# Kernel tuning notes

Measured on AMD Instinct MI355X. Metric: run time of the kernel, lower is better.

## Reference

```python
import jax, jax.numpy as jnp
import numpy as np

B, T, D, H, E = 2, 1024, 1024, 4096, 8


def setup_inputs() -> dict:
    key = jax.random.key(0)
    ks = jax.random.split(key, 7)
    s = 0.02  # weight init scale
    return {
        "x": jax.random.normal(ks[0], (B, T, D), jnp.float32),
        "gate_w": jax.random.normal(ks[1], (D, E), jnp.float32) * s,
        "gate_b": jnp.zeros((E,), jnp.float32),
        "w1": jax.random.normal(ks[2], (E, D, H), jnp.float32) * s,
        "b1": jnp.zeros((E, H), jnp.float32),
        "w2": jax.random.normal(ks[3], (E, H, D), jnp.float32) * s,
        "b2": jnp.zeros((E, D), jnp.float32),
    }


def reference(x, gate_w, gate_b, w1, b1, w2, b2):
    b, t, d = x.shape
    e = gate_w.shape[1]
    xt = x.reshape(b * t, d)                      # [N, D]
    logits = xt @ gate_w + gate_b                 # [N, E]
    probs = jax.nn.softmax(logits, axis=-1)
    top_expert = jnp.argmax(probs, axis=-1)       # [N]
    onehot = jax.nn.one_hot(top_expert, e, dtype=x.dtype)  # [N, E]
    # dense per-expert FFN, then combine via top-1 one-hot (same math as masked dispatch)
    h = jax.nn.gelu(jnp.einsum('nd,edh->enh', xt, w1) + b1[:, None, :], approximate=False)  # [E, N, H]
    y = jnp.einsum('enh,ehd->end', h, w2) + b2[:, None, :]                                  # [E, N, D]
    out = jnp.einsum('end,ne->nd', y, onehot).reshape(b, t, d)
    counts = jnp.sum(onehot, axis=0)              # [E], float
    frac = counts / jnp.maximum(counts.sum(), 1.0)
    aux_loss = jnp.mean((frac - 1.0 / e) ** 2)
    return out, aux_loss
```

## Files before the change

kernel.cpp:

```cpp
#include <hip/hip_runtime.h>
#include <stdint.h>

#define N_TOK 2048
#define DDIM 1024
#define HDIM 4096
#define NEXP 8
#define BM 256
#define MAXT 16
#define ACAP 2560

#define C_COUNTS 0
#define C_CURSOR 8
#define C_PADOFF 16
#define C_TILECNT 25
#define C_TILE_E 32
#define C_TILE_M0 56
#define C_TILE_ROWS 80
#define C_EXPERT 128
#define C_PERM 2176

#define XG_OFF 32768
#define HG_OFF (XG_OFF + ACAP*DDIM*2)

typedef float f32x4 __attribute__((ext_vector_type(4)));
typedef short s16x8 __attribute__((ext_vector_type(8)));
typedef unsigned int u32;
typedef u32 u32x2 __attribute__((ext_vector_type(2)));
typedef unsigned short u16;

__device__ __forceinline__ u16 f2bf(float f){
  u32 u = __float_as_uint(f);
  u += 0x7fffu + ((u >> 16) & 1u);
  return (u16)(u >> 16);
}

__device__ __forceinline__ u32 pkbf(float a, float b){
  u32 r; asm("v_cvt_pk_bf16_f32 %0, %1, %2" : "=v"(r) : "v"(a), "v"(b)); return r;
}

__device__ __forceinline__ void gl_lds16(const void* g, void* l){
  __builtin_amdgcn_global_load_lds((const __attribute__((address_space(1))) u32*)g,
                                   (__attribute__((address_space(3))) u32*)l, 16, 0, 0);
}

__global__ __launch_bounds__(256) void gate_kern(
    const float* __restrict__ x, const float* __restrict__ gw,
    const float* __restrict__ gb, int* __restrict__ ctrl)
{
  const int wv = threadIdx.x >> 6, l = threadIdx.x & 63;
  const int n = blockIdx.x * 4 + wv;
  const float* xr = x + (size_t)n * DDIM;
  float acc[NEXP];
  #pragma unroll
  for (int e = 0; e < NEXP; e++) acc[e] = 0.f;
  #pragma unroll 4
  for (int i = 0; i < DDIM/64; i++){
    int k = i*64 + l;
    float xv = xr[k];
    const float* g = gw + (size_t)k * NEXP;
    #pragma unroll
    for (int e = 0; e < NEXP; e++) acc[e] = fmaf(xv, g[e], acc[e]);
  }
  #pragma unroll
  for (int e = 0; e < NEXP; e++){
    #pragma unroll
    for (int off = 32; off > 0; off >>= 1) acc[e] += __shfl_xor(acc[e], off);
  }
  if (l == 0){
    float best = acc[0] + gb[0]; int bi = 0;
    #pragma unroll
    for (int e = 1; e < NEXP; e++){
      float v = acc[e] + gb[e];
      if (v > best){ best = v; bi = e; }
    }
    ctrl[C_EXPERT + n] = bi;
    atomicAdd(&ctrl[C_COUNTS + bi], 1);
  }
}

__global__ void setup_kern(int* __restrict__ ctrl, float* __restrict__ aux_out)
{
  const int t = threadIdx.x;
  for (int i = t; i < 3072; i += 256) ctrl[C_PERM + i] = -1;
  if (t == 0){
    int off = 0, tc = 0;
    float aux = 0.f;
    for (int e = 0; e < NEXP; e++){
      int c = ctrl[C_COUNTS + e];
      ctrl[C_PADOFF + e] = off;
      ctrl[C_CURSOR + e] = off;
      int nt = (c + BM - 1) / BM;
      for (int j = 0; j < nt; j++){
        ctrl[C_TILE_E   + tc] = e;
        ctrl[C_TILE_M0  + tc] = off + j*BM;
        ctrl[C_TILE_ROWS+ tc] = min(BM, c - j*BM);
        tc++;
      }
      off += c;
      float fr = (float)c * (1.f/(float)N_TOK);
      float d = fr - 1.f/(float)NEXP;
      aux += d*d;
    }
    ctrl[C_TILECNT] = tc;
    *aux_out = aux * (1.f/(float)NEXP);
  }
}

__global__ __launch_bounds__(256) void scatter_kern(int* __restrict__ ctrl)
{
  const int n = blockIdx.x * 256 + threadIdx.x;
  const int e = ctrl[C_EXPERT + n];
  const int pos = atomicAdd(&ctrl[C_CURSOR + e], 1);
  ctrl[C_PERM + pos] = n;
}

__global__ __launch_bounds__(256) void xg_kern(
    const float* __restrict__ x, const int* __restrict__ ctrl,
    u16* __restrict__ Xg)
{
  const int slot = blockIdx.x, t = threadIdx.x;
  const int tok = ctrl[C_PERM + slot];
  ushort4 o;
  if (tok >= 0){
    f32x4 v = *(const f32x4*)(x + (size_t)tok*DDIM + t*4);
    o.x = f2bf(v.x); o.y = f2bf(v.y); o.z = f2bf(v.z); o.w = f2bf(v.w);
  } else { o.x = 0; o.y = 0; o.z = 0; o.w = 0; }
  *(ushort4*)(Xg + (size_t)slot*DDIM + t*4) = o;
}

template<int MODE>
__global__ __launch_bounds__(512, 2) void moe_gemm(
    const u16* __restrict__ Ag, const float* __restrict__ W,
    const float* __restrict__ bias, u16* __restrict__ Hg,
    float* __restrict__ outp, const int* __restrict__ ctrl)
{
  constexpr int K    = (MODE==1) ? DDIM : HDIM;
  constexpr int NN   = (MODE==1) ? HDIM : DDIM;
  constexpr int KS   = (MODE==1) ? 1 : 4;
  constexpr int KLOC = K / KS;
  constexpr int BN   = 128;
  constexpr int BK   = 32;
  constexpr int NT   = KLOC / BK;

  const int by = blockIdx.y;
  if (by >= ctrl[C_TILECNT]) return;
  const int e    = ctrl[C_TILE_E + by];
  const int m0   = ctrl[C_TILE_M0 + by];
  const int rows = ctrl[C_TILE_ROWS + by];
  const int n0   = blockIdx.x * BN;
  const int kb   = (MODE==1) ? 0 : blockIdx.z * KLOC;

  const int tid = threadIdx.x;
  const int w = tid >> 6, l = tid & 63;
  const int wr = w >> 1, wc = w & 1;
  const int lhi = l >> 4, llo = l & 15;

  __shared__ __align__(16) u16 As[2][BM*BK];
  __shared__ __align__(16) u16 Bs[2][BN*BK];
  __shared__ int perm_s[BM];

  if constexpr (MODE == 2){
    if (tid < BM) perm_s[tid] = ctrl[C_PERM + m0 + tid];
  }

  f32x4 acc[4][4];
  #pragma unroll
  for (int mf = 0; mf < 4; mf++)
    #pragma unroll
    for (int nf = 0; nf < 4; nf++) acc[mf][nf] = (f32x4){0.f,0.f,0.f,0.f};

  const u16* Abase = Ag + (size_t)m0 * K;
  int arow[2], apos[2];
  #pragma unroll
  for (int i = 0; i < 2; i++){
    int f = i*512 + tid;
    arow[i] = f >> 2;
    apos[i] = (f & 3) ^ (arow[i] & 3) ^ (((arow[i] >> 2) & 1) << 1);
  }
  const int bn  = tid & 127;
  const int bkg = tid >> 7;
  const int bsw = (bn >> 1) & 7;
  const float* Wn = W + (size_t)e * K * NN + n0 + bn;
  float wreg[8];

#define STAGE_A(buf, k0) { \
    u16* ad = &As[buf][(w*64)*8]; \
    _Pragma("unroll") \
    for (int i = 0; i < 2; i++) \
      gl_lds16(Abase + (size_t)arow[i]*K + (k0) + apos[i]*8, ad + i*512*8); }

#define BLOAD(k0) { \
    _Pragma("unroll") \
    for (int i = 0; i < 8; i++) \
      wreg[i] = Wn[(size_t)((k0) + bkg*8 + i) * NN]; }

#define BPACK(buf) { \
    u32 p0 = pkbf(wreg[0], wreg[1]), p1 = pkbf(wreg[2], wreg[3]); \
    u32 p2 = pkbf(wreg[4], wreg[5]), p3 = pkbf(wreg[6], wreg[7]); \
    u16* bd = &Bs[buf][bn*BK]; \
    *(u32x2*)&bd[((2*bkg)   ^ bsw) << 2] = (u32x2){p0, p1}; \
    *(u32x2*)&bd[((2*bkg+1) ^ bsw) << 2] = (u32x2){p2, p3}; }

#define COMPUTE(buf) { \
    s16x8 a[4]; \
    _Pragma("unroll") \
    for (int mf = 0; mf < 4; mf++){ \
      int row = wr*64 + mf*16 + llo; \
      int pos = (lhi ^ (row & 3)) ^ (((row >> 2) & 1) << 1); \
      a[mf] = *(const s16x8*)&As[buf][row*BK + pos*8]; } \
    _Pragma("unroll") \
    for (int nf = 0; nf < 4; nf++){ \
      const int col = wc*64 + nf*16 + llo; \
      const int sw = (col >> 1) & 7; \
      const u16* bb = &Bs[buf][col*BK]; \
      union { u32 u[4]; s16x8 v; } bfr; \
      *(u32x2*)&bfr.u[0] = *(const u32x2*)&bb[((2*lhi)   ^ sw) << 2]; \
      *(u32x2*)&bfr.u[2] = *(const u32x2*)&bb[((2*lhi+1) ^ sw) << 2]; \
      _Pragma("unroll") \
      for (int mf = 0; mf < 4; mf++) \
        acc[mf][nf] = __builtin_amdgcn_mfma_f32_16x16x32_bf16(a[mf], bfr.v, acc[mf][nf], 0, 0, 0); \
    } }

  BLOAD(kb);
  STAGE_A(0, kb);
  BPACK(0);
  __syncthreads();

  int cur = 0;
  #pragma unroll 1
  for (int t = 0; t < NT; t++){
    if (t+1 < NT){
      BLOAD(kb + (t+1)*BK);
      STAGE_A(cur^1, kb + (t+1)*BK);
    }
    COMPUTE(cur);
    if (t+1 < NT){ BPACK(cur^1); }
    __syncthreads();
    cur ^= 1;
  }

  if constexpr (MODE == 1){
    const float* bp = bias + (size_t)e*NN + n0;
    #pragma unroll
    for (int nf = 0; nf < 4; nf++){
      const int cl = wc*64 + nf*16 + llo;
      const float bb = bp[cl];
      #pragma unroll
      for (int mf = 0; mf < 4; mf++){
        #pragma unroll
        for (int r = 0; r < 4; r++){
          const int rl = wr*64 + mf*16 + lhi*4 + r;
          if (rl < rows){
            float vv = acc[mf][nf][r] + bb;
            float gel = 0.5f * vv * (1.0f + erff(vv * 0.70710678118f));
            Hg[(size_t)(m0+rl)*NN + n0 + cl] = f2bf(gel);
          }
        }
      }
    }
  } else {
    const float* bp = bias + (size_t)e*NN + n0;
    const bool addb = (blockIdx.z == 0);
    #pragma unroll
    for (int mf = 0; mf < 4; mf++){
      #pragma unroll
      for (int r = 0; r < 4; r++){
        const int rl = wr*64 + mf*16 + lhi*4 + r;
        if (rl < rows){
          const int tok = perm_s[rl];
          #pragma unroll
          for (int nf = 0; nf < 4; nf++){
            const int cl = wc*64 + nf*16 + llo;
            float v = acc[mf][nf][r] + (addb ? bp[cl] : 0.f);
            atomicAdd(&outp[(size_t)tok*DDIM + n0 + cl], v);
          }
        }
      }
    }
  }
#undef STAGE_A
#undef BLOAD
#undef BPACK
#undef COMPUTE
}

extern "C" void kernel_launch(void* const* d_in, const int* in_sizes, int n_in,
                              void* d_out, int out_size, void* d_ws, size_t ws_size,
                              hipStream_t stream)
{
  (void)in_sizes; (void)n_in; (void)out_size; (void)ws_size;
  const float* x  = (const float*)d_in[0];
  const float* gw = (const float*)d_in[1];
  const float* gb = (const float*)d_in[2];
  const float* w1 = (const float*)d_in[3];
  const float* b1 = (const float*)d_in[4];
  const float* w2 = (const float*)d_in[5];
  const float* b2 = (const float*)d_in[6];
  float* out = (float*)d_out;
  char* ws = (char*)d_ws;
  int* ctrl = (int*)ws;
  u16* Xg = (u16*)(ws + XG_OFF);
  u16* Hg = (u16*)(ws + HG_OFF);

  hipMemsetAsync(ctrl, 0, 64, stream);
  hipMemsetAsync(out, 0, (size_t)N_TOK*DDIM*4, stream);
  gate_kern<<<N_TOK/4, 256, 0, stream>>>(x, gw, gb, ctrl);
  setup_kern<<<1, 256, 0, stream>>>(ctrl, out + (size_t)N_TOK*DDIM);
  scatter_kern<<<N_TOK/256, 256, 0, stream>>>(ctrl);
  xg_kern<<<N_TOK, 256, 0, stream>>>(x, ctrl, Xg);
  moe_gemm<1><<<dim3(HDIM/128, MAXT),    512, 0, stream>>>(Xg, w1, b1, Hg, nullptr, ctrl);
  moe_gemm<2><<<dim3(DDIM/128, MAXT, 4), 512, 0, stream>>>(Hg, w2, b2, nullptr, out, ctrl);
}
```

Baseline: 216.4 us.

## Pre-convert expert weights to transposed bf16 and use 128-row GEMM tiles

Adds a kernel that converts and transposes all fp32 expert weights into bf16 in workspace every call, so the GEMMs can stream weights with direct global-to-LDS copies and no per-tile fp32-to-bf16 packing. The GEMM tile shrinks to 128 rows with BK=64 and 256 threads, giving more tiles per expert. The new path runs only when the workspace is large enough, otherwise it falls back to the old fp32-weight kernels. The conversion reads all 256 MB of fp32 weights and writes 128 MB of bf16 each call, so total weight traffic rises unless the GEMMs get much cheaper.

New measurement: 285.6 us. 32.0% more time.

```diff
diff --git a/kernel.cpp b/kernel.cpp
--- a/kernel.cpp
+++ b/kernel.cpp
@@ -5,9 +5,6 @@
 #define DDIM 1024
 #define HDIM 4096
 #define NEXP 8
-#define BM 256
-#define MAXT 16
-#define ACAP 2560
 
 #define C_COUNTS 0
 #define C_CURSOR 8
@@ -19,8 +16,16 @@
 #define C_EXPERT 128
 #define C_PERM 2176
 
-#define XG_OFF 32768
-#define HG_OFF (XG_OFF + ACAP*DDIM*2)
+#define ACAPB 2304
+#define XGB_OFF 32768
+#define HGB_OFF (XGB_OFF + ACAPB*DDIM*2)
+#define W1B_OFF (HGB_OFF + ACAPB*HDIM*2)
+#define W2B_OFF (W1B_OFF + (size_t)NEXP*DDIM*HDIM*2)
+#define WS_NEED (W2B_OFF + (size_t)NEXP*HDIM*DDIM*2)
+
+#define ACAP2 2560
+#define XG2_OFF 32768
+#define HG2_OFF (XG2_OFF + ACAP2*DDIM*2)
 
 typedef float f32x4 __attribute__((ext_vector_type(4)));
 typedef short s16x8 __attribute__((ext_vector_type(8)));
@@ -78,7 +83,8 @@
   }
 }
 
-__global__ void setup_kern(int* __restrict__ ctrl, float* __restrict__ aux_out)
+__global__ void setup_kern(int* __restrict__ ctrl, float* __restrict__ aux_out,
+                           int bm)
 {
   const int t = threadIdx.x;
   for (int i = t; i < 3072; i += 256) ctrl[C_PERM + i] = -1;
@@ -89,11 +95,11 @@
       int c = ctrl[C_COUNTS + e];
       ctrl[C_PADOFF + e] = off;
       ctrl[C_CURSOR + e] = off;
-      int nt = (c + BM - 1) / BM;
+      int nt = (c + bm - 1) / bm;
       for (int j = 0; j < nt; j++){
         ctrl[C_TILE_E   + tc] = e;
-        ctrl[C_TILE_M0  + tc] = off + j*BM;
-        ctrl[C_TILE_ROWS+ tc] = min(BM, c - j*BM);
+        ctrl[C_TILE_M0  + tc] = off + j*bm;
+        ctrl[C_TILE_ROWS+ tc] = min(bm, c - j*bm);
         tc++;
       }
       off += c;
@@ -128,18 +134,52 @@
   *(ushort4*)(Xg + (size_t)slot*DDIM + t*4) = o;
 }
 
+__global__ __launch_bounds__(256) void wconv_kern(
+    const float* __restrict__ src, u16* __restrict__ dst, int K, int NN)
+{
+  const int TN = NN >> 6, TK = K >> 6;
+  int b = blockIdx.x;
+  const int e  = b / (TK*TN); b -= e*TK*TN;
+  const int kt = b / TN;
+  const int nt = b - kt*TN;
+  const int t = threadIdx.x;
+
+  __shared__ float ld[64][67];
+
+  const float* S = src + (size_t)e*K*NN + (size_t)(kt*64)*NN + nt*64;
+  #pragma unroll
+  for (int p = 0; p < 4; p++){
+    int kr = p*16 + (t >> 4);
+    int nc = (t & 15) * 4;
+    f32x4 v = *(const f32x4*)(S + (size_t)kr*NN + nc);
+    ld[kr][nc+0] = v.x; ld[kr][nc+1] = v.y; ld[kr][nc+2] = v.z; ld[kr][nc+3] = v.w;
+  }
+  __syncthreads();
+
+  u16* D = dst + (size_t)e*NN*K + (size_t)(nt*64)*K + kt*64;
+  #pragma unroll
+  for (int q = 0; q < 2; q++){
+    int s = q*256 + t;
+    int n = s >> 3, kc = s & 7;
+    union { u32 u[4]; } o;
+    #pragma unroll
+    for (int j = 0; j < 4; j++)
+      o.u[j] = pkbf(ld[kc*8 + 2*j][n], ld[kc*8 + 2*j + 1][n]);
+    *(u32x2*)(D + (size_t)n*K + kc*8)     = (u32x2){o.u[0], o.u[1]};
+    *(u32x2*)(D + (size_t)n*K + kc*8 + 4) = (u32x2){o.u[2], o.u[3]};
+  }
+}
+
 template<int MODE>
-__global__ __launch_bounds__(512, 2) void moe_gemm(
-    const u16* __restrict__ Ag, const float* __restrict__ W,
+__global__ __launch_bounds__(256, 2) void moe_gemm_bf(
+    const u16* __restrict__ Ag, const u16* __restrict__ Wt,
     const float* __restrict__ bias, u16* __restrict__ Hg,
     float* __restrict__ outp, const int* __restrict__ ctrl)
 {
   constexpr int K    = (MODE==1) ? DDIM : HDIM;
   constexpr int NN   = (MODE==1) ? HDIM : DDIM;
-  constexpr int KS   = (MODE==1) ? 1 : 4;
-  constexpr int KLOC = K / KS;
-  constexpr int BN   = 128;
-  constexpr int BK   = 32;
+  constexpr int KLOC = 1024;
+  constexpr int BK   = 64;
   constexpr int NT   = KLOC / BK;
 
   const int by = blockIdx.y;
@@ -147,7 +187,7 @@
   const int e    = ctrl[C_TILE_E + by];
   const int m0   = ctrl[C_TILE_M0 + by];
   const int rows = ctrl[C_TILE_ROWS + by];
-  const int n0   = blockIdx.x * BN;
+  const int n0   = blockIdx.x * 128;
   const int kb   = (MODE==1) ? 0 : blockIdx.z * KLOC;
 
   const int tid = threadIdx.x;
@@ -155,12 +195,146 @@
   const int wr = w >> 1, wc = w & 1;
   const int lhi = l >> 4, llo = l & 15;
 
-  __shared__ __align__(16) u16 As[2][BM*BK];
-  __shared__ __align__(16) u16 Bs[2][BN*BK];
-  __shared__ int perm_s[BM];
+  __shared__ __align__(16) u16 As[2][128*BK];
+  __shared__ __align__(16) u16 Bs[2][128*BK];
+  __shared__ int perm_s[128];
 
   if constexpr (MODE == 2){
-    if (tid < BM) perm_s[tid] = ctrl[C_PERM + m0 + tid];
+    if (tid < 128) perm_s[tid] = ctrl[C_PERM + m0 + tid];
+  }
+
+  f32x4 acc[4][4];
+  #pragma unroll
+  for (int mf = 0; mf < 4; mf++)
+    #pragma unroll
+    for (int nf = 0; nf < 4; nf++) acc[mf][nf] = (f32x4){0.f,0.f,0.f,0.f};
+
+  const u16* Abase = Ag + (size_t)m0 * K;
+  const u16* Bbase = Wt + (size_t)e * NN * K + (size_t)n0 * K;
+  int grow[4], gpos[4];
+  #pragma unroll
+  for (int i = 0; i < 4; i++){
+    int f = i*256 + tid;
+    grow[i] = f >> 3;
+    gpos[i] = (f & 7) ^ (grow[i] & 7);
+  }
+
+#define STAGE(buf, k0) { \
+    u16* ad = &As[buf][(w*64)*8]; \
+    u16* bd = &Bs[buf][(w*64)*8]; \
+    _Pragma("unroll") \
+    for (int i = 0; i < 4; i++){ \
+      gl_lds16(Abase + (size_t)grow[i]*K + (k0) + gpos[i]*8, ad + i*256*8); \
+      gl_lds16(Bbase + (size_t)grow[i]*K + (k0) + gpos[i]*8, bd + i*256*8); } }
+
+#define COMPUTE(buf) { \
+    _Pragma("unroll") \
+    for (int kk = 0; kk < 2; kk++){ \
+      s16x8 a[4], b[4]; \
+      _Pragma("unroll") \
+      for (int mf = 0; mf < 4; mf++){ \
+        int row = wr*64 + mf*16 + llo; \
+        int pos = ((kk<<2) | lhi) ^ (row & 7); \
+        a[mf] = *(const s16x8*)&As[buf][row*BK + pos*8]; } \
+      _Pragma("unroll") \
+      for (int nf = 0; nf < 4; nf++){ \
+        int col = wc*64 + nf*16 + llo; \
+        int pos = ((kk<<2) | lhi) ^ (col & 7); \
+        b[nf] = *(const s16x8*)&Bs[buf][col*BK + pos*8]; } \
+      _Pragma("unroll") \
+      for (int mf = 0; mf < 4; mf++) \
+        _Pragma("unroll") \
+        for (int nf = 0; nf < 4; nf++) \
+          acc[mf][nf] = __builtin_amdgcn_mfma_f32_16x16x32_bf16(a[mf], b[nf], acc[mf][nf], 0, 0, 0); } }
+
+  STAGE(0, kb);
+  __syncthreads();
+
+  int cur = 0;
+  #pragma unroll 1
+  for (int t = 0; t < NT; t++){
+    if (t+1 < NT){ STAGE(cur^1, kb + (t+1)*BK); }
+    COMPUTE(cur);
+    __syncthreads();
+    cur ^= 1;
+  }
+
+  if constexpr (MODE == 1){
+    const float* bp = bias + (size_t)e*NN + n0;
+    #pragma unroll
+    for (int nf = 0; nf < 4; nf++){
+      const int cl = wc*64 + nf*16 + llo;
+      const float bb = bp[cl];
+      #pragma unroll
+      for (int mf = 0; mf < 4; mf++){
+        #pragma unroll
+        for (int r = 0; r < 4; r++){
+          const int rl = wr*64 + mf*16 + lhi*4 + r;
+          if (rl < rows){
+            float vv = acc[mf][nf][r] + bb;
+            float gel = 0.5f * vv * (1.0f + erff(vv * 0.70710678118f));
+            Hg[(size_t)(m0+rl)*NN + n0 + cl] = f2bf(gel);
+          }
+        }
+      }
+    }
+  } else {
+    const float* bp = bias + (size_t)e*NN + n0;
+    const bool addb = (blockIdx.z == 0);
+    #pragma unroll
+    for (int mf = 0; mf < 4; mf++){
+      #pragma unroll
+      for (int r = 0; r < 4; r++){
+        const int rl = wr*64 + mf*16 + lhi*4 + r;
+        if (rl < rows){
+          const int tok = perm_s[rl];
+          #pragma unroll
+          for (int nf = 0; nf < 4; nf++){
+            const int cl = wc*64 + nf*16 + llo;
+            float v = acc[mf][nf][r] + (addb ? bp[cl] : 0.f);
+            atomicAdd(&outp[(size_t)tok*DDIM + n0 + cl], v);
+          }
+        }
+      }
+    }
+  }
+#undef STAGE
+#undef COMPUTE
+}
+
+template<int MODE>
+__global__ __launch_bounds__(512, 2) void moe_gemm_f32(
+    const u16* __restrict__ Ag, const float* __restrict__ W,
+    const float* __restrict__ bias, u16* __restrict__ Hg,
+    float* __restrict__ outp, const int* __restrict__ ctrl)
+{
+  constexpr int K    = (MODE==1) ? DDIM : HDIM;
+  constexpr int NN   = (MODE==1) ? HDIM : DDIM;
+  constexpr int KS   = (MODE==1) ? 1 : 4;
+  constexpr int KLOC = K / KS;
+  constexpr int BM2  = 256;
+  constexpr int BK   = 32;
+  constexpr int NT   = KLOC / BK;
+
+  const int by = blockIdx.y;
+  if (by >= ctrl[C_TILECNT]) return;
+  const int e    = ctrl[C_TILE_E + by];
+  const int m0   = ctrl[C_TILE_M0 + by];
+  const int rows = ctrl[C_TILE_ROWS + by];
+  const int n0   = blockIdx.x * 128;
+  const int kb   = (MODE==1) ? 0 : blockIdx.z * KLOC;
+
+  const int tid = threadIdx.x;
+  const int w = tid >> 6, l = tid & 63;
+  const int wr = w >> 1, wc = w & 1;
+  const int lhi = l >> 4, llo = l & 15;
+
+  __shared__ __align__(16) u16 As[2][BM2*BK];
+  __shared__ __align__(16) u16 Bs[2][128*BK];
+  __shared__ int perm_s[BM2];
+
+  if constexpr (MODE == 2){
+    if (tid < BM2) perm_s[tid] = ctrl[C_PERM + m0 + tid];
   }
 
   f32x4 acc[4][4];
@@ -288,7 +462,7 @@
                               void* d_out, int out_size, void* d_ws, size_t ws_size,
                               hipStream_t stream)
 {
-  (void)in_sizes; (void)n_in; (void)out_size; (void)ws_size;
+  (void)in_sizes; (void)n_in; (void)out_size;
   const float* x  = (const float*)d_in[0];
   const float* gw = (const float*)d_in[1];
   const float* gb = (const float*)d_in[2];
@@ -299,15 +473,30 @@
   float* out = (float*)d_out;
   char* ws = (char*)d_ws;
   int* ctrl = (int*)ws;
-  u16* Xg = (u16*)(ws + XG_OFF);
-  u16* Hg = (u16*)(ws + HG_OFF);
+
+  const bool wb = (ws_size >= (size_t)WS_NEED);
 
   hipMemsetAsync(ctrl, 0, 64, stream);
   hipMemsetAsync(out, 0, (size_t)N_TOK*DDIM*4, stream);
   gate_kern<<<N_TOK/4, 256, 0, stream>>>(x, gw, gb, ctrl);
-  setup_kern<<<1, 256, 0, stream>>>(ctrl, out + (size_t)N_TOK*DDIM);
+  setup_kern<<<1, 256, 0, stream>>>(ctrl, out + (size_t)N_TOK*DDIM, wb ? 128 : 256);
   scatter_kern<<<N_TOK/256, 256, 0, stream>>>(ctrl);
-  xg_kern<<<N_TOK, 256, 0, stream>>>(x, ctrl, Xg);
-  moe_gemm<1><<<dim3(HDIM/128, MAXT),    512, 0, stream>>>(Xg, w1, b1, Hg, nullptr, ctrl);
-  moe_gemm<2><<<dim3(DDIM/128, MAXT, 4), 512, 0, stream>>>(Hg, w2, b2, nullptr, out, ctrl);
-}
+
+  if (wb){
+    u16* Xg  = (u16*)(ws + XGB_OFF);
+    u16* Hg  = (u16*)(ws + HGB_OFF);
+    u16* W1b = (u16*)(ws + W1B_OFF);
+    u16* W2b = (u16*)(ws + W2B_OFF);
+    xg_kern<<<N_TOK, 256, 0, stream>>>(x, ctrl, Xg);
+    wconv_kern<<<NEXP*(DDIM/64)*(HDIM/64), 256, 0, stream>>>(w1, W1b, DDIM, HDIM);
+    wconv_kern<<<NEXP*(HDIM/64)*(DDIM/64), 256, 0, stream>>>(w2, W2b, HDIM, DDIM);
+    moe_gemm_bf<1><<<dim3(HDIM/128, 24),    256, 0, stream>>>(Xg, W1b, b1, Hg, nullptr, ctrl);
+    moe_gemm_bf<2><<<dim3(DDIM/128, 24, 4), 256, 0, stream>>>(Hg, W2b, b2, nullptr, out, ctrl);
+  } else {
+    u16* Xg = (u16*)(ws + XG2_OFF);
+    u16* Hg = (u16*)(ws + HG2_OFF);
+    xg_kern<<<N_TOK, 256, 0, stream>>>(x, ctrl, Xg);
+    moe_gemm_f32<1><<<dim3(HDIM/128, 16),    512, 0, stream>>>(Xg, w1, b1, Hg, nullptr, ctrl);
+    moe_gemm_f32<2><<<dim3(DDIM/128, 16, 4), 512, 0, stream>>>(Hg, w2, b2, nullptr, out, ctrl);
+  }
+}
```
